# Optimization experiments

Hardware: AMD Instinct MI355X
Metric: run time of the kernel (lower is better)

The kernel has to match this reference:

```python
import jax, jax.numpy as jnp
import numpy as np

B, S, D = 4, 2048, 1024
H, HK = 16, 4          # num_heads, num_heads_kv
HD = D // H            # head_dim = 64
G = H // HK            # kv groups = 4


def setup_inputs() -> dict:
    key = jax.random.key(0)
    ks = jax.random.split(key, 7)
    s = 0.02
    return {
        "query": jax.random.normal(ks[0], (B, S, D), jnp.float32),
        "key":   jax.random.normal(ks[1], (B, S, D), jnp.float32),
        "value": jax.random.normal(ks[2], (B, S, D), jnp.float32),
        # weights stored (in, out); equivalent to torch Linear y = x @ W.T
        "Wq": jax.random.normal(ks[3], (D, H * HD), jnp.float32) * s,
        "Wk": jax.random.normal(ks[4], (D, HK * HD), jnp.float32) * s,
        "Wv": jax.random.normal(ks[5], (D, HK * HD), jnp.float32) * s,
        "Wo": jax.random.normal(ks[6], (H * HD, D), jnp.float32) * s,
    }


def reference(query, key, value, Wq, Wk, Wv, Wo):
    b, qlen, _ = query.shape
    kvlen = key.shape[1]
    # projections
    q = (query @ Wq).reshape(b, qlen, H, HD)        # [b,q,H,hd]
    k = (key @ Wk).reshape(b, kvlen, HK, HD)        # [b,s,HK,hd]
    v = (value @ Wv).reshape(b, kvlen, HK, HD)      # [b,s,HK,hd]
    # GQA: q head h attends kv head h//G (repeat_interleave semantics)
    qg = q.reshape(b, qlen, HK, G, HD)              # head = kv*G + group
    scale = 1.0 / jnp.sqrt(jnp.asarray(HD, q.dtype))
    # scores [b,HK,G,q,s] -- broadcast kv heads, no materialized repeat
    scores = jnp.einsum('bqkgd,bskd->bkgqs', qg, k) * scale
    attn = jax.nn.softmax(scores, axis=-1)
    out = jnp.einsum('bkgqs,bskd->bqkgd', attn, v)  # [b,q,HK,G,hd]
    out = out.reshape(b, qlen, H * HD)
    return out @ Wo
```

## Files before the change

### kernel.cpp

```cpp
#include <hip/hip_runtime.h>


typedef unsigned short u16;
typedef unsigned int   u32;
typedef __bf16 bf16x4 __attribute__((ext_vector_type(4)));
typedef __bf16 bf16x8 __attribute__((ext_vector_type(8)));
typedef float  f32x4  __attribute__((ext_vector_type(4)));

#define MFMA(a,b,c) __builtin_amdgcn_mfma_f32_16x16x32_bf16((a),(b),(c),0,0,0)

#define GLDS(g, l) __builtin_amdgcn_global_load_lds(                          \
    (const __attribute__((address_space(1))) void*)(g),                       \
    (__attribute__((address_space(3))) void*)(l), 16, 0, 0)

__device__ __forceinline__ u16 f2bf(float f){
    u32 u = __builtin_bit_cast(u32, f);
    u += 0x7fffu + ((u >> 16) & 1u);
    return (u16)(u >> 16);
}
__device__ __forceinline__ u32 pk2(float a, float b){
#if __has_builtin(__builtin_amdgcn_cvt_pk_bf16_f32)
    auto r = __builtin_amdgcn_cvt_pk_bf16_f32(a, b);
    return __builtin_bit_cast(u32, r);
#else
    return (u32)f2bf(a) | ((u32)f2bf(b) << 16);
#endif
}
__device__ __forceinline__ u16 cvt1(float a){ return (u16)pk2(a, 0.f); }

__device__ __forceinline__ bf16x8 ldfrag(const u16* p){
    return *(const bf16x8*)p;
}
__device__ __forceinline__ bf16x8 ld2x64(const u16* p){
    bf16x4 lo = *(const bf16x4*)p;
    bf16x4 hi = *(const bf16x4*)(p + 4);
    bf16x8 r;
    r[0]=lo[0]; r[1]=lo[1]; r[2]=lo[2]; r[3]=lo[3];
    r[4]=hi[0]; r[5]=hi[1]; r[6]=hi[2]; r[7]=hi[3];
    return r;
}

__device__ __forceinline__ void wcast_body(const float* __restrict__ W,
                                           u16* __restrict__ WT, int K, int N){
    __shared__ float T[32][33];
    int kt = blockIdx.x * 32, nt = blockIdx.y * 32;
    if (nt >= N) return;
    int r = threadIdx.x >> 3, c = threadIdx.x & 7;
    float4 v = *(const float4*)(W + (size_t)(kt + r) * N + nt + c * 4);
    T[r][c*4+0] = v.x; T[r][c*4+1] = v.y; T[r][c*4+2] = v.z; T[r][c*4+3] = v.w;
    __syncthreads();
    u32 lo = pk2(T[c*4+0][r], T[c*4+1][r]);
    u32 hi = pk2(T[c*4+2][r], T[c*4+3][r]);
    *(uint2*)(WT + (size_t)(nt + r) * K + kt + c * 4) = make_uint2(lo, hi);
}
__global__ __launch_bounds__(256) void wcast4(const float* W0, const float* W1,
                                              const float* W2, const float* W3,
                                              u16* T0, u16* T1, u16* T2, u16* T3){
    switch (blockIdx.z){
        case 0: wcast_body(W0, T0, 1024, 1024); break;
        case 1: wcast_body(W1, T1, 1024,  256); break;
        case 2: wcast_body(W2, T2, 1024,  256); break;
        default: wcast_body(W3, T3, 1024, 1024); break;
    }
}

template<int ATYPE, int EPI>
__device__ __forceinline__ void gemm_body(const void* __restrict__ Ap,
                                          const u16* __restrict__ Bt,
                                          void* __restrict__ Cp,
                                          int N, int K, int m0, int n0,
                                          u16* As, u16* Bs, float oscale){
    constexpr int ASTR = (ATYPE == 0) ? 80 : 64;
    const int tid  = threadIdx.x;
    const int wave = tid >> 6, lane = tid & 63;
    const int quad = lane >> 4, l15 = lane & 15;
    const int wm = wave >> 1, wn = wave & 1;

    f32x4 acc[4][4];
    #pragma unroll
    for (int i = 0; i < 4; ++i)
        #pragma unroll
        for (int j = 0; j < 4; ++j) acc[i][j] = (f32x4){0.f, 0.f, 0.f, 0.f};

    const int nkt = K >> 6;
    for (int kt = 0; kt < nkt; ++kt){
        __syncthreads();
        if constexpr (ATYPE == 0){
            const float* A = (const float*)Ap;
            int c4 = tid & 15, r0 = tid >> 4;
            #pragma unroll
            for (int p = 0; p < 8; ++p){
                int r = r0 + p * 16;
                float4 v = *(const float4*)(A + (size_t)(m0 + r) * K + kt * 64 + c4 * 4);
                *(uint2*)&As[r * 80 + c4 * 4] = make_uint2(pk2(v.x, v.y), pk2(v.z, v.w));
            }
        } else {
            const u16* A = (const u16*)Ap;
            const u16* ga = A + (size_t)(m0 + wave*32 + (lane>>3)) * K + kt*64 + (lane&7)*8;
            u16* la = As + (wave*32) * 64;
            #pragma unroll
            for (int p = 0; p < 4; ++p)
                GLDS(ga + (size_t)(p*8) * K, la + p*8*64);
        }
        {
            const u16* gb = Bt + (size_t)(n0 + wave*32 + (lane>>3)) * K + kt*64 + (lane&7)*8;
            u16* lb = Bs + (wave*32) * 64;
            #pragma unroll
            for (int p = 0; p < 4; ++p)
                GLDS(gb + (size_t)(p*8) * K, lb + p*8*64);
        }
        __syncthreads();
        #pragma unroll
        for (int ks = 0; ks < 2; ++ks){
            bf16x8 af[4], bfr[4];
            #pragma unroll
            for (int mt = 0; mt < 4; ++mt)
                af[mt] = ldfrag(&As[(wm*64 + mt*16 + l15) * ASTR + ks*32 + quad*8]);
            #pragma unroll
            for (int nt = 0; nt < 4; ++nt)
                bfr[nt] = ldfrag(&Bs[(wn*64 + nt*16 + l15) * 64 + ks*32 + quad*8]);
            #pragma unroll
            for (int mt = 0; mt < 4; ++mt)
                #pragma unroll
                for (int nt = 0; nt < 4; ++nt)
                    acc[mt][nt] = MFMA(af[mt], bfr[nt], acc[mt][nt]);
        }
    }
    #pragma unroll
    for (int mt = 0; mt < 4; ++mt){
        int rowb = m0 + wm*64 + mt*16 + quad*4;
        #pragma unroll
        for (int nt = 0; nt < 4; ++nt){
            int col = n0 + wn*64 + nt*16 + l15;
            if constexpr (EPI == 0){
                u16* C = (u16*)Cp;
                #pragma unroll
                for (int r = 0; r < 4; ++r)
                    C[(size_t)(rowb + r) * N + col] = cvt1(acc[mt][nt][r] * oscale);
            } else if constexpr (EPI == 2){
                float* C = (float*)Cp;
                #pragma unroll
                for (int r = 0; r < 4; ++r)
                    C[(size_t)(rowb + r) * N + col] = acc[mt][nt][r];
            } else {
                u16* C = (u16*)Cp;
                int bb = rowb >> 11, s = rowb & 2047;
                u32 lo = pk2(acc[mt][nt][0], acc[mt][nt][1]);
                u32 hi = pk2(acc[mt][nt][2], acc[mt][nt][3]);
                *(uint2*)(C + (size_t)(bb * 256 + col) * 2048 + s) = make_uint2(lo, hi);
            }
        }
    }
}

template<int ATYPE, int EPI>
__global__ __launch_bounds__(256) void gemm_k(const void* __restrict__ Ap,
                                              const u16* __restrict__ Bt,
                                              void* __restrict__ Cp,
                                              int N, int K, float oscale){
    __shared__ u16 As[128 * ((ATYPE == 0) ? 80 : 64)];
    __shared__ u16 Bs[128 * 64];
    gemm_body<ATYPE, EPI>(Ap, Bt, Cp, N, K, blockIdx.y * 128, blockIdx.x * 128,
                          As, Bs, oscale);
}

__global__ __launch_bounds__(256) void gemm_kv(const void* __restrict__ key,
                                               const u16* __restrict__ WkT,
                                               void* __restrict__ Kp,
                                               const void* __restrict__ value,
                                               const u16* __restrict__ WvT,
                                               void* __restrict__ Vt){
    __shared__ u16 As[128 * 80];
    __shared__ u16 Bs[128 * 64];
    if (blockIdx.z == 0)
        gemm_body<0,0>(key,   WkT, Kp, 256, 1024, blockIdx.y * 128, blockIdx.x * 128,
                       As, Bs, 1.0f);
    else
        gemm_body<0,1>(value, WvT, Vt, 256, 1024, blockIdx.y * 128, blockIdx.x * 128,
                       As, Bs, 1.0f);
}

__global__ __launch_bounds__(256, 4) void attn_k(const u16* __restrict__ Qp,
                                                 const u16* __restrict__ Kp,
                                                 const u16* __restrict__ Vt,
                                                 u16* __restrict__ AO){
    constexpr int S = 2048, Dm = 1024, NKV = 256, HD = 64;
    __shared__ u16 Ks[64 * 72];
    __shared__ u16 Vs[64 * 72];
    __shared__ u16 Ps[4 * 32 * 68];
    const int tid = threadIdx.x, wave = tid >> 6, lane = tid & 63;
    const int quad = lane >> 4, l15 = lane & 15;
    const int qt = blockIdx.x, h = blockIdx.y, b = blockIdx.z;
    const int hk = h >> 2, q0 = qt * 128;
    u16* pw = Ps + wave * (32 * 68);

    {
        int c8 = tid & 7, r0 = tid >> 3;
        #pragma unroll
        for (int p = 0; p < 4; ++p){
            int r = r0 + p * 32;
            uint4 v = *(const uint4*)(Qp + (size_t)(b * S + q0 + r) * Dm + h * HD + c8 * 8);
            *(uint2*)&Ps[r * 68 + c8 * 8]     = make_uint2(v.x, v.y);
            *(uint2*)&Ps[r * 68 + c8 * 8 + 4] = make_uint2(v.z, v.w);
        }
    }
    __syncthreads();
    bf16x8 qf[2][2];
    #pragma unroll
    for (int mt = 0; mt < 2; ++mt)
        #pragma unroll
        for (int ks = 0; ks < 2; ++ks)
            qf[mt][ks] = ld2x64(&Ps[(wave*32 + mt*16 + l15) * 68 + ks*32 + quad*8]);

    f32x4 O[2][4];
    #pragma unroll
    for (int mt = 0; mt < 2; ++mt)
        #pragma unroll
        for (int nt = 0; nt < 4; ++nt) O[mt][nt] = (f32x4){0.f, 0.f, 0.f, 0.f};
    float psum[2][4];
    #pragma unroll
    for (int mt = 0; mt < 2; ++mt)
        #pragma unroll
        for (int r = 0; r < 4; ++r) psum[mt][r] = 0.f;

    for (int t = 0; t < 32; ++t){
        int j0 = t * 64;
        __syncthreads();
        {
            int c8 = tid & 7, r0 = tid >> 3;
            #pragma unroll
            for (int p = 0; p < 2; ++p){
                int r = r0 + p * 32;
                *(uint4*)&Ks[r * 72 + c8 * 8] =
                    *(const uint4*)(Kp + (size_t)(b * S + j0 + r) * NKV + hk * HD + c8 * 8);
                *(uint4*)&Vs[r * 72 + c8 * 8] =
                    *(const uint4*)(Vt + (size_t)(b * NKV + hk * HD + r) * S + j0 + c8 * 8);
            }
        }
        __syncthreads();
        f32x4 sf[2][4];
        #pragma unroll
        for (int mt = 0; mt < 2; ++mt)
            #pragma unroll
            for (int nt = 0; nt < 4; ++nt) sf[mt][nt] = (f32x4){0.f, 0.f, 0.f, 0.f};
        #pragma unroll
        for (int ks = 0; ks < 2; ++ks){
            #pragma unroll
            for (int nt = 0; nt < 4; ++nt){
                bf16x8 bk = ldfrag(&Ks[(nt*16 + l15) * 72 + ks*32 + quad*8]);
                #pragma unroll
                for (int mt = 0; mt < 2; ++mt)
                    sf[mt][nt] = MFMA(qf[mt][ks], bk, sf[mt][nt]);
            }
        }
        #pragma unroll
        for (int mt = 0; mt < 2; ++mt)
            #pragma unroll
            for (int nt = 0; nt < 4; ++nt)
                #pragma unroll
                for (int r = 0; r < 4; ++r){
                    float e = exp2f(sf[mt][nt][r]);
                    psum[mt][r] += e;
                    pw[(mt*16 + quad*4 + r) * 68 + nt*16 + l15] = cvt1(e);
                }
        __threadfence_block();
        #pragma unroll
        for (int ks = 0; ks < 2; ++ks){
            bf16x8 ap[2];
            #pragma unroll
            for (int mt = 0; mt < 2; ++mt)
                ap[mt] = ld2x64(&pw[(mt*16 + l15) * 68 + ks*32 + quad*8]);
            #pragma unroll
            for (int nt = 0; nt < 4; ++nt){
                bf16x8 bv = ldfrag(&Vs[(nt*16 + l15) * 72 + ks*32 + quad*8]);
                #pragma unroll
                for (int mt = 0; mt < 2; ++mt)
                    O[mt][nt] = MFMA(ap[mt], bv, O[mt][nt]);
            }
        }
    }
    #pragma unroll
    for (int mt = 0; mt < 2; ++mt)
        #pragma unroll
        for (int r = 0; r < 4; ++r){
            float v = psum[mt][r];
            v += __shfl_xor(v, 1); v += __shfl_xor(v, 2);
            v += __shfl_xor(v, 4); v += __shfl_xor(v, 8);
            psum[mt][r] = 1.0f / v;
        }
    #pragma unroll
    for (int mt = 0; mt < 2; ++mt)
        #pragma unroll
        for (int r = 0; r < 4; ++r){
            int row = b * S + q0 + wave*32 + mt*16 + quad*4 + r;
            #pragma unroll
            for (int nt = 0; nt < 4; ++nt)
                AO[(size_t)row * Dm + h * HD + nt*16 + l15] =
                    cvt1(O[mt][nt][r] * psum[mt][r]);
        }
}

extern "C" void kernel_launch(void* const* d_in, const int* in_sizes, int n_in,
                              void* d_out, int out_size, void* d_ws, size_t ws_size,
                              hipStream_t stream){
    const float* q  = (const float*)d_in[0];
    const float* k  = (const float*)d_in[1];
    const float* v  = (const float*)d_in[2];
    const float* Wq = (const float*)d_in[3];
    const float* Wk = (const float*)d_in[4];
    const float* Wv = (const float*)d_in[5];
    const float* Wo = (const float*)d_in[6];
    char* ws = (char*)d_ws;
    u16* WqT = (u16*)(ws);
    u16* WkT = (u16*)(ws + (size_t)(2u  << 20));
    u16* WvT = (u16*)(ws + (size_t)(2560u << 10));
    u16* WoT = (u16*)(ws + (size_t)(3u  << 20));
    u16* Qp  = (u16*)(ws + (size_t)(5u  << 20));
    u16* Kp  = (u16*)(ws + (size_t)(21u << 20));
    u16* Vt  = (u16*)(ws + (size_t)(25u << 20));
    u16* AO  = (u16*)(ws + (size_t)(29u << 20));

    const float cexp = 0.125f * 1.44269504f;

    wcast4<<<dim3(32, 32, 4), 256, 0, stream>>>(Wq, Wk, Wv, Wo, WqT, WkT, WvT, WoT);

    gemm_k<0,0><<<dim3(8, 64), 256, 0, stream>>>((const void*)q, WqT, (void*)Qp,
                                                 1024, 1024, cexp);
    gemm_kv<<<dim3(2, 64, 2), 256, 0, stream>>>((const void*)k, WkT, (void*)Kp,
                                                (const void*)v, WvT, (void*)Vt);

    attn_k<<<dim3(16, 16, 4), 256, 0, stream>>>(Qp, Kp, Vt, AO);

    gemm_k<1,2><<<dim3(8, 64), 256, 0, stream>>>((const void*)AO, WoT, d_out,
                                                 1024, 1024, 1.0f);
}
```

Before: 351.2 us.

## Pre-cast activations to bf16, merge QKV GEMMs, prefetch K/V and transpose MFMA outputs

A single prep kernel now casts the weights and the fp32 q/k/v activations to bf16, so every GEMM can use async global-to-LDS loads. The Q, K and V projections run in one merged launch. The GEMM and attention MFMAs swap their operand order so each lane holds contiguous output columns, which allows vectorized stores and a cheaper row-sum reduction. The attention loop register-prefetches the next K/V tile and uses the hardware exp2 builtin. The trade is an extra full read and write pass over the activations in the prep kernel, and AO now reuses the Qc buffer.

```diff
diff --git a/kernel.cpp b/kernel.cpp
--- a/kernel.cpp
+++ b/kernel.cpp
@@ -12,6 +12,12 @@
 #define GLDS(g, l) __builtin_amdgcn_global_load_lds(                          \
     (const __attribute__((address_space(1))) void*)(g),                       \
     (__attribute__((address_space(3))) void*)(l), 16, 0, 0)
+
+#if __has_builtin(__builtin_amdgcn_exp2f)
+#define EXP2(x) __builtin_amdgcn_exp2f(x)
+#else
+#define EXP2(x) exp2f(x)
+#endif
 
 __device__ __forceinline__ u16 f2bf(float f){
     u32 u = __builtin_bit_cast(u32, f);
@@ -26,8 +32,6 @@
     return (u32)f2bf(a) | ((u32)f2bf(b) << 16);
 #endif
 }
-__device__ __forceinline__ u16 cvt1(float a){ return (u16)pk2(a, 0.f); }
-
 __device__ __forceinline__ bf16x8 ldfrag(const u16* p){
     return *(const bf16x8*)p;
 }
@@ -40,37 +44,53 @@
     return r;
 }
 
-__device__ __forceinline__ void wcast_body(const float* __restrict__ W,
-                                           u16* __restrict__ WT, int K, int N){
-    __shared__ float T[32][33];
-    int kt = blockIdx.x * 32, nt = blockIdx.y * 32;
-    if (nt >= N) return;
-    int r = threadIdx.x >> 3, c = threadIdx.x & 7;
-    float4 v = *(const float4*)(W + (size_t)(kt + r) * N + nt + c * 4);
-    T[r][c*4+0] = v.x; T[r][c*4+1] = v.y; T[r][c*4+2] = v.z; T[r][c*4+3] = v.w;
-    __syncthreads();
-    u32 lo = pk2(T[c*4+0][r], T[c*4+1][r]);
-    u32 hi = pk2(T[c*4+2][r], T[c*4+3][r]);
-    *(uint2*)(WT + (size_t)(nt + r) * K + kt + c * 4) = make_uint2(lo, hi);
-}
-__global__ __launch_bounds__(256) void wcast4(const float* W0, const float* W1,
-                                              const float* W2, const float* W3,
-                                              u16* T0, u16* T1, u16* T2, u16* T3){
-    switch (blockIdx.z){
-        case 0: wcast_body(W0, T0, 1024, 1024); break;
-        case 1: wcast_body(W1, T1, 1024,  256); break;
-        case 2: wcast_body(W2, T2, 1024,  256); break;
-        default: wcast_body(W3, T3, 1024, 1024); break;
-    }
-}
-
-template<int ATYPE, int EPI>
-__device__ __forceinline__ void gemm_body(const void* __restrict__ Ap,
+__global__ __launch_bounds__(256) void prep(const float* __restrict__ q,
+                                            const float* __restrict__ k,
+                                            const float* __restrict__ v,
+                                            const float* __restrict__ Wq,
+                                            const float* __restrict__ Wk,
+                                            const float* __restrict__ Wv,
+                                            const float* __restrict__ Wo,
+                                            u16* Qc, u16* Kc, u16* Vc,
+                                            u16* WqT, u16* WkT, u16* WvT, u16* WoT){
+    const int tid = threadIdx.x, bid = blockIdx.x;
+    if (bid < 2560){
+        __shared__ float T[32][33];
+        const float* W; u16* WT; int N, i;
+        if (bid < 1024)      { W = Wq; WT = WqT; N = 1024; i = bid; }
+        else if (bid < 1280) { W = Wk; WT = WkT; N =  256; i = bid - 1024; }
+        else if (bid < 1536) { W = Wv; WT = WvT; N =  256; i = bid - 1280; }
+        else                 { W = Wo; WT = WoT; N = 1024; i = bid - 1536; }
+        int kt = (i & 31) * 32, nt = (i >> 5) * 32;
+        int r = tid >> 3, c = tid & 7;
+        float4 vv = *(const float4*)(W + (size_t)(kt + r) * N + nt + c * 4);
+        T[r][c*4+0] = vv.x; T[r][c*4+1] = vv.y; T[r][c*4+2] = vv.z; T[r][c*4+3] = vv.w;
+        __syncthreads();
+        u32 lo = pk2(T[c*4+0][r], T[c*4+1][r]);
+        u32 hi = pk2(T[c*4+2][r], T[c*4+3][r]);
+        *(uint2*)(WT + (size_t)(nt + r) * 1024 + kt + c * 4) = make_uint2(lo, hi);
+    } else {
+        int i = bid - 2560;
+        const float* src = (i < 512) ? q : (i < 1024 ? k : v);
+        u16*         dst = (i < 512) ? Qc : (i < 1024 ? Kc : Vc);
+        size_t off = (size_t)(i & 511) * 16384;
+        const float* s = src + off;
+        u16* d = dst + off;
+        #pragma unroll
+        for (int p = 0; p < 16; ++p){
+            int idx = (p * 256 + tid) * 4;
+            float4 vv = *(const float4*)(s + idx);
+            *(uint2*)(d + idx) = make_uint2(pk2(vv.x, vv.y), pk2(vv.z, vv.w));
+        }
+    }
+}
+
+template<int EPI>
+__device__ __forceinline__ void gemm_body(const u16* __restrict__ A,
                                           const u16* __restrict__ Bt,
                                           void* __restrict__ Cp,
                                           int N, int K, int m0, int n0,
                                           u16* As, u16* Bs, float oscale){
-    constexpr int ASTR = (ATYPE == 0) ? 80 : 64;
     const int tid  = threadIdx.x;
     const int wave = tid >> 6, lane = tid & 63;
     const int quad = lane >> 4, l15 = lane & 15;
@@ -85,24 +105,12 @@
     const int nkt = K >> 6;
     for (int kt = 0; kt < nkt; ++kt){
         __syncthreads();
-        if constexpr (ATYPE == 0){
-            const float* A = (const float*)Ap;
-            int c4 = tid & 15, r0 = tid >> 4;
-            #pragma unroll
-            for (int p = 0; p < 8; ++p){
-                int r = r0 + p * 16;
-                float4 v = *(const float4*)(A + (size_t)(m0 + r) * K + kt * 64 + c4 * 4);
-                *(uint2*)&As[r * 80 + c4 * 4] = make_uint2(pk2(v.x, v.y), pk2(v.z, v.w));
-            }
-        } else {
-            const u16* A = (const u16*)Ap;
+        {
             const u16* ga = A + (size_t)(m0 + wave*32 + (lane>>3)) * K + kt*64 + (lane&7)*8;
             u16* la = As + (wave*32) * 64;
             #pragma unroll
             for (int p = 0; p < 4; ++p)
                 GLDS(ga + (size_t)(p*8) * K, la + p*8*64);
-        }
-        {
             const u16* gb = Bt + (size_t)(n0 + wave*32 + (lane>>3)) * K + kt*64 + (lane&7)*8;
             u16* lb = Bs + (wave*32) * 64;
             #pragma unroll
@@ -115,76 +123,85 @@
             bf16x8 af[4], bfr[4];
             #pragma unroll
             for (int mt = 0; mt < 4; ++mt)
-                af[mt] = ldfrag(&As[(wm*64 + mt*16 + l15) * ASTR + ks*32 + quad*8]);
+                af[mt] = ldfrag(&As[(wm*64 + mt*16 + l15) * 64 + ks*32 + quad*8]);
             #pragma unroll
             for (int nt = 0; nt < 4; ++nt)
                 bfr[nt] = ldfrag(&Bs[(wn*64 + nt*16 + l15) * 64 + ks*32 + quad*8]);
             #pragma unroll
             for (int mt = 0; mt < 4; ++mt)
                 #pragma unroll
-                for (int nt = 0; nt < 4; ++nt)
-                    acc[mt][nt] = MFMA(af[mt], bfr[nt], acc[mt][nt]);
+                for (int nt = 0; nt < 4; ++nt){
+                    if constexpr (EPI == 1)
+                        acc[mt][nt] = MFMA(af[mt], bfr[nt], acc[mt][nt]);
+                    else
+                        acc[mt][nt] = MFMA(bfr[nt], af[mt], acc[mt][nt]);
+                }
         }
     }
     #pragma unroll
     for (int mt = 0; mt < 4; ++mt){
-        int rowb = m0 + wm*64 + mt*16 + quad*4;
         #pragma unroll
         for (int nt = 0; nt < 4; ++nt){
-            int col = n0 + wn*64 + nt*16 + l15;
-            if constexpr (EPI == 0){
-                u16* C = (u16*)Cp;
-                #pragma unroll
-                for (int r = 0; r < 4; ++r)
-                    C[(size_t)(rowb + r) * N + col] = cvt1(acc[mt][nt][r] * oscale);
-            } else if constexpr (EPI == 2){
-                float* C = (float*)Cp;
-                #pragma unroll
-                for (int r = 0; r < 4; ++r)
-                    C[(size_t)(rowb + r) * N + col] = acc[mt][nt][r];
-            } else {
+            if constexpr (EPI == 1){
+                int rowb = m0 + wm*64 + mt*16 + quad*4;
+                int col  = n0 + wn*64 + nt*16 + l15;
                 u16* C = (u16*)Cp;
                 int bb = rowb >> 11, s = rowb & 2047;
                 u32 lo = pk2(acc[mt][nt][0], acc[mt][nt][1]);
                 u32 hi = pk2(acc[mt][nt][2], acc[mt][nt][3]);
                 *(uint2*)(C + (size_t)(bb * 256 + col) * 2048 + s) = make_uint2(lo, hi);
+            } else {
+                int row  = m0 + wm*64 + mt*16 + l15;
+                int colb = n0 + wn*64 + nt*16 + quad*4;
+                if constexpr (EPI == 0){
+                    u16* C = (u16*)Cp;
+                    u32 lo = pk2(acc[mt][nt][0]*oscale, acc[mt][nt][1]*oscale);
+                    u32 hi = pk2(acc[mt][nt][2]*oscale, acc[mt][nt][3]*oscale);
+                    *(uint2*)(C + (size_t)row * N + colb) = make_uint2(lo, hi);
+                } else {
+                    float* C = (float*)Cp;
+                    *(f32x4*)(C + (size_t)row * N + colb) = acc[mt][nt];
+                }
             }
         }
     }
 }
 
-template<int ATYPE, int EPI>
-__global__ __launch_bounds__(256) void gemm_k(const void* __restrict__ Ap,
-                                              const u16* __restrict__ Bt,
-                                              void* __restrict__ Cp,
-                                              int N, int K, float oscale){
-    __shared__ u16 As[128 * ((ATYPE == 0) ? 80 : 64)];
+__global__ __launch_bounds__(256) void gemm_qkv(const u16* Qc, const u16* WqT, u16* Qp,
+                                                const u16* Kc, const u16* WkT, u16* Kp,
+                                                const u16* Vc, const u16* WvT, u16* Vt,
+                                                float qscale){
+    __shared__ u16 As[128 * 64];
     __shared__ u16 Bs[128 * 64];
-    gemm_body<ATYPE, EPI>(Ap, Bt, Cp, N, K, blockIdx.y * 128, blockIdx.x * 128,
-                          As, Bs, oscale);
-}
-
-__global__ __launch_bounds__(256) void gemm_kv(const void* __restrict__ key,
-                                               const u16* __restrict__ WkT,
-                                               void* __restrict__ Kp,
-                                               const void* __restrict__ value,
-                                               const u16* __restrict__ WvT,
-                                               void* __restrict__ Vt){
-    __shared__ u16 As[128 * 80];
+    int bid = blockIdx.x;
+    if (bid < 512)
+        gemm_body<0>(Qc, WqT, Qp, 1024, 1024, (bid >> 3) * 128, (bid & 7) * 128,
+                     As, Bs, qscale);
+    else if (bid < 640){
+        int i = bid - 512;
+        gemm_body<0>(Kc, WkT, Kp, 256, 1024, (i >> 1) * 128, (i & 1) * 128,
+                     As, Bs, 1.0f);
+    } else {
+        int i = bid - 640;
+        gemm_body<1>(Vc, WvT, Vt, 256, 1024, (i >> 1) * 128, (i & 1) * 128,
+                     As, Bs, 1.0f);
+    }
+}
+
+__global__ __launch_bounds__(256) void gemm_o(const u16* AO, const u16* WoT,
+                                              float* Out){
+    __shared__ u16 As[128 * 64];
     __shared__ u16 Bs[128 * 64];
-    if (blockIdx.z == 0)
-        gemm_body<0,0>(key,   WkT, Kp, 256, 1024, blockIdx.y * 128, blockIdx.x * 128,
-                       As, Bs, 1.0f);
-    else
-        gemm_body<0,1>(value, WvT, Vt, 256, 1024, blockIdx.y * 128, blockIdx.x * 128,
-                       As, Bs, 1.0f);
+    int bid = blockIdx.x;
+    gemm_body<2>(AO, WoT, Out, 1024, 1024, (bid >> 3) * 128, (bid & 7) * 128,
+                 As, Bs, 1.0f);
 }
 
 __global__ __launch_bounds__(256, 4) void attn_k(const u16* __restrict__ Qp,
                                                  const u16* __restrict__ Kp,
                                                  const u16* __restrict__ Vt,
                                                  u16* __restrict__ AO){
-    constexpr int S = 2048, Dm = 1024, NKV = 256, HD = 64;
+    constexpr int S = 2048, Dm = 1024, NKV = 256;
     __shared__ u16 Ks[64 * 72];
     __shared__ u16 Vs[64 * 72];
     __shared__ u16 Ps[4 * 32 * 68];
@@ -192,14 +209,14 @@
     const int quad = lane >> 4, l15 = lane & 15;
     const int qt = blockIdx.x, h = blockIdx.y, b = blockIdx.z;
     const int hk = h >> 2, q0 = qt * 128;
+    const int c8 = tid & 7, r0 = tid >> 3;
     u16* pw = Ps + wave * (32 * 68);
 
     {
-        int c8 = tid & 7, r0 = tid >> 3;
         #pragma unroll
         for (int p = 0; p < 4; ++p){
             int r = r0 + p * 32;
-            uint4 v = *(const uint4*)(Qp + (size_t)(b * S + q0 + r) * Dm + h * HD + c8 * 8);
+            uint4 v = *(const uint4*)(Qp + (size_t)(b * S + q0 + r) * Dm + h * 64 + c8 * 8);
             *(uint2*)&Ps[r * 68 + c8 * 8]     = make_uint2(v.x, v.y);
             *(uint2*)&Ps[r * 68 + c8 * 8 + 4] = make_uint2(v.z, v.w);
         }
@@ -212,92 +229,103 @@
         for (int ks = 0; ks < 2; ++ks)
             qf[mt][ks] = ld2x64(&Ps[(wave*32 + mt*16 + l15) * 68 + ks*32 + quad*8]);
 
-    f32x4 O[2][4];
-    #pragma unroll
-    for (int mt = 0; mt < 2; ++mt)
-        #pragma unroll
-        for (int nt = 0; nt < 4; ++nt) O[mt][nt] = (f32x4){0.f, 0.f, 0.f, 0.f};
-    float psum[2][4];
-    #pragma unroll
-    for (int mt = 0; mt < 2; ++mt)
-        #pragma unroll
-        for (int r = 0; r < 4; ++r) psum[mt][r] = 0.f;
+    f32x4 O[4][2];
+    #pragma unroll
+    for (int dt = 0; dt < 4; ++dt)
+        #pragma unroll
+        for (int mt = 0; mt < 2; ++mt) O[dt][mt] = (f32x4){0.f, 0.f, 0.f, 0.f};
+    float psum[2] = {0.f, 0.f};
+
+    uint4 kpre[2], vpre[2];
+    #pragma unroll
+    for (int p = 0; p < 2; ++p){
+        int r = r0 + p * 32;
+        kpre[p] = *(const uint4*)(Kp + (size_t)(b * S + r) * NKV + hk * 64 + c8 * 8);
+        vpre[p] = *(const uint4*)(Vt + (size_t)(b * NKV + hk * 64 + r) * S + c8 * 8);
+    }
 
     for (int t = 0; t < 32; ++t){
-        int j0 = t * 64;
-        __syncthreads();
-        {
-            int c8 = tid & 7, r0 = tid >> 3;
+        __syncthreads();
+        #pragma unroll
+        for (int p = 0; p < 2; ++p){
+            int r = r0 + p * 32;
+            *(uint4*)&Ks[r * 72 + c8 * 8] = kpre[p];
+            *(uint4*)&Vs[r * 72 + c8 * 8] = vpre[p];
+        }
+        __syncthreads();
+        if (t < 31){
+            int j0n = (t + 1) * 64;
             #pragma unroll
             for (int p = 0; p < 2; ++p){
                 int r = r0 + p * 32;
-                *(uint4*)&Ks[r * 72 + c8 * 8] =
-                    *(const uint4*)(Kp + (size_t)(b * S + j0 + r) * NKV + hk * HD + c8 * 8);
-                *(uint4*)&Vs[r * 72 + c8 * 8] =
-                    *(const uint4*)(Vt + (size_t)(b * NKV + hk * HD + r) * S + j0 + c8 * 8);
+                kpre[p] = *(const uint4*)(Kp + (size_t)(b * S + j0n + r) * NKV + hk * 64 + c8 * 8);
+                vpre[p] = *(const uint4*)(Vt + (size_t)(b * NKV + hk * 64 + r) * S + j0n + c8 * 8);
             }
         }
-        __syncthreads();
-        f32x4 sf[2][4];
-        #pragma unroll
-        for (int mt = 0; mt < 2; ++mt)
-            #pragma unroll
-            for (int nt = 0; nt < 4; ++nt) sf[mt][nt] = (f32x4){0.f, 0.f, 0.f, 0.f};
+        f32x4 sf[4][2];
+        #pragma unroll
+        for (int nt = 0; nt < 4; ++nt)
+            #pragma unroll
+            for (int mt = 0; mt < 2; ++mt) sf[nt][mt] = (f32x4){0.f, 0.f, 0.f, 0.f};
         #pragma unroll
         for (int ks = 0; ks < 2; ++ks){
-            #pragma unroll
-            for (int nt = 0; nt < 4; ++nt){
-                bf16x8 bk = ldfrag(&Ks[(nt*16 + l15) * 72 + ks*32 + quad*8]);
+            bf16x8 ak[4];
+            #pragma unroll
+            for (int nt = 0; nt < 4; ++nt)
+                ak[nt] = ldfrag(&Ks[(nt*16 + l15) * 72 + ks*32 + quad*8]);
+            #pragma unroll
+            for (int nt = 0; nt < 4; ++nt)
                 #pragma unroll
                 for (int mt = 0; mt < 2; ++mt)
-                    sf[mt][nt] = MFMA(qf[mt][ks], bk, sf[mt][nt]);
+                    sf[nt][mt] = MFMA(ak[nt], qf[mt][ks], sf[nt][mt]);
+        }
+        #pragma unroll
+        for (int mt = 0; mt < 2; ++mt)
+            #pragma unroll
+            for (int nt = 0; nt < 4; ++nt){
+                float e0 = EXP2(sf[nt][mt][0]);
+                float e1 = EXP2(sf[nt][mt][1]);
+                float e2 = EXP2(sf[nt][mt][2]);
+                float e3 = EXP2(sf[nt][mt][3]);
+                psum[mt] += (e0 + e1) + (e2 + e3);
+                *(uint2*)&pw[(mt*16 + l15) * 68 + nt*16 + quad*4] =
+                    make_uint2(pk2(e0, e1), pk2(e2, e3));
             }
-        }
-        #pragma unroll
-        for (int mt = 0; mt < 2; ++mt)
-            #pragma unroll
-            for (int nt = 0; nt < 4; ++nt)
-                #pragma unroll
-                for (int r = 0; r < 4; ++r){
-                    float e = exp2f(sf[mt][nt][r]);
-                    psum[mt][r] += e;
-                    pw[(mt*16 + quad*4 + r) * 68 + nt*16 + l15] = cvt1(e);
-                }
         __threadfence_block();
         #pragma unroll
         for (int ks = 0; ks < 2; ++ks){
-            bf16x8 ap[2];
+            bf16x8 av[4], bp[2];
+            #pragma unroll
+            for (int dt = 0; dt < 4; ++dt)
+                av[dt] = ldfrag(&Vs[(dt*16 + l15) * 72 + ks*32 + quad*8]);
             #pragma unroll
             for (int mt = 0; mt < 2; ++mt)
-                ap[mt] = ld2x64(&pw[(mt*16 + l15) * 68 + ks*32 + quad*8]);
-            #pragma unroll
-            for (int nt = 0; nt < 4; ++nt){
-                bf16x8 bv = ldfrag(&Vs[(nt*16 + l15) * 72 + ks*32 + quad*8]);
+                bp[mt] = ld2x64(&pw[(mt*16 + l15) * 68 + ks*32 + quad*8]);
+            #pragma unroll
+            for (int dt = 0; dt < 4; ++dt)
                 #pragma unroll
                 for (int mt = 0; mt < 2; ++mt)
-                    O[mt][nt] = MFMA(ap[mt], bv, O[mt][nt]);
-            }
-        }
-    }
-    #pragma unroll
-    for (int mt = 0; mt < 2; ++mt)
-        #pragma unroll
-        for (int r = 0; r < 4; ++r){
-            float v = psum[mt][r];
-            v += __shfl_xor(v, 1); v += __shfl_xor(v, 2);
-            v += __shfl_xor(v, 4); v += __shfl_xor(v, 8);
-            psum[mt][r] = 1.0f / v;
-        }
-    #pragma unroll
-    for (int mt = 0; mt < 2; ++mt)
-        #pragma unroll
-        for (int r = 0; r < 4; ++r){
-            int row = b * S + q0 + wave*32 + mt*16 + quad*4 + r;
-            #pragma unroll
-            for (int nt = 0; nt < 4; ++nt)
-                AO[(size_t)row * Dm + h * HD + nt*16 + l15] =
-                    cvt1(O[mt][nt][r] * psum[mt][r]);
-        }
+                    O[dt][mt] = MFMA(av[dt], bp[mt], O[dt][mt]);
+        }
+    }
+    float inv[2];
+    #pragma unroll
+    for (int mt = 0; mt < 2; ++mt){
+        float v = psum[mt];
+        v += __shfl_xor(v, 16);
+        v += __shfl_xor(v, 32);
+        inv[mt] = 1.0f / v;
+    }
+    #pragma unroll
+    for (int mt = 0; mt < 2; ++mt){
+        size_t row = (size_t)(b * S + q0 + wave*32 + mt*16 + l15);
+        #pragma unroll
+        for (int dt = 0; dt < 4; ++dt){
+            u32 lo = pk2(O[dt][mt][0] * inv[mt], O[dt][mt][1] * inv[mt]);
+            u32 hi = pk2(O[dt][mt][2] * inv[mt], O[dt][mt][3] * inv[mt]);
+            *(uint2*)(AO + row * Dm + h * 64 + dt*16 + quad*4) = make_uint2(lo, hi);
+        }
+    }
 }
 
 extern "C" void kernel_launch(void* const* d_in, const int* in_sizes, int n_in,
@@ -311,26 +339,25 @@
     const float* Wv = (const float*)d_in[5];
     const float* Wo = (const float*)d_in[6];
     char* ws = (char*)d_ws;
+    const size_t MB = 1u << 20;
     u16* WqT = (u16*)(ws);
-    u16* WkT = (u16*)(ws + (size_t)(2u  << 20));
-    u16* WvT = (u16*)(ws + (size_t)(2560u << 10));
-    u16* WoT = (u16*)(ws + (size_t)(3u  << 20));
-    u16* Qp  = (u16*)(ws + (size_t)(5u  << 20));
-    u16* Kp  = (u16*)(ws + (size_t)(21u << 20));
-    u16* Vt  = (u16*)(ws + (size_t)(25u << 20));
-    u16* AO  = (u16*)(ws + (size_t)(29u << 20));
+    u16* WkT = (u16*)(ws + 2*MB);
+    u16* WvT = (u16*)(ws + 2*MB + 512*1024);
+    u16* WoT = (u16*)(ws + 3*MB);
+    u16* Qc  = (u16*)(ws + 5*MB);
+    u16* Kc  = (u16*)(ws + 21*MB);
+    u16* Vc  = (u16*)(ws + 37*MB);
+    u16* Qp  = (u16*)(ws + 53*MB);
+    u16* Kp  = (u16*)(ws + 69*MB);
+    u16* Vt  = (u16*)(ws + 73*MB);
+    u16* AO  = (u16*)(ws + 5*MB);
 
     const float cexp = 0.125f * 1.44269504f;
 
-    wcast4<<<dim3(32, 32, 4), 256, 0, stream>>>(Wq, Wk, Wv, Wo, WqT, WkT, WvT, WoT);
-
-    gemm_k<0,0><<<dim3(8, 64), 256, 0, stream>>>((const void*)q, WqT, (void*)Qp,
-                                                 1024, 1024, cexp);
-    gemm_kv<<<dim3(2, 64, 2), 256, 0, stream>>>((const void*)k, WkT, (void*)Kp,
-                                                (const void*)v, WvT, (void*)Vt);
-
+    prep<<<dim3(4096), 256, 0, stream>>>(q, k, v, Wq, Wk, Wv, Wo,
+                                         Qc, Kc, Vc, WqT, WkT, WvT, WoT);
+    gemm_qkv<<<dim3(768), 256, 0, stream>>>(Qc, WqT, Qp, Kc, WkT, Kp,
+                                            Vc, WvT, Vt, cexp);
     attn_k<<<dim3(16, 16, 4), 256, 0, stream>>>(Qp, Kp, Vt, AO);
-
-    gemm_k<1,2><<<dim3(8, 64), 256, 0, stream>>>((const void*)AO, WoT, d_out,
-                                                 1024, 1024, 1.0f);
-}
+    gemm_o<<<dim3(512), 256, 0, stream>>>(AO, WoT, (float*)d_out);
+}
```

Result: slower. 426.4 us (+21.4%).
